# Kernel optimization log

Hardware: AMD Instinct MI355X
Metric: run time of the kernel (lower is better)

## Reference

```python
import jax, jax.numpy as jnp
import numpy as np

N_CELLS = 4096          # rows of sparse x
N_INPUT_GENES = 20000   # cols of sparse x == len(input_gene_list)
N_PRETRAINED = 30000    # rows of embedding table
NUM_HID = 128
NNZ = 2097152           # ~512 expressed genes per cell


def setup_inputs() -> dict:
    key = jax.random.key(0)
    k_val, k_row, k_col, k_gidx, k_emb = jax.random.split(key, 5)
    x_values = jax.random.uniform(k_val, (NNZ,), dtype=jnp.float32)
    x_rows = jnp.sort(jax.random.randint(k_row, (NNZ,), 0, N_CELLS))
    x_cols = jax.random.randint(k_col, (NNZ,), 0, N_INPUT_GENES)
    gene_idx = jax.random.randint(k_gidx, (N_INPUT_GENES,), 0, N_PRETRAINED)
    # nn.Parameter(torch.randn(...) * 0.005)
    embs = jax.random.normal(k_emb, (N_PRETRAINED, NUM_HID), dtype=jnp.float32) * 0.005
    return {"x_values": x_values, "x_rows": x_rows, "x_cols": x_cols,
            "gene_idx": gene_idx, "embs": embs}


def reference(x_values, x_rows, x_cols, gene_idx, embs):
    # feat = F.embedding(gene_idx, embs)           -> [G_in, H]
    # out  = torch.sparse.mm(x, feat)              -> [N_cells, H]
    # Fused: gather per-nnz embedding rows, scale by value, segment-sum by cell.
    feat = embs[gene_idx]                                   # [G_in, H]
    contrib = x_values[:, None] * feat[x_cols]              # [NNZ, H]
    out = jax.ops.segment_sum(contrib, x_rows,
                              num_segments=N_CELLS,
                              indices_are_sorted=True)      # [N_cells, H]
    return out
```

## Files before the change

kernel.cpp:

```cpp
#include <hip/hip_runtime.h>

#define NNZ_TOT    2097152
#define N_CELLS    4096
#define N_GIN      20000
#define N_PRE      30000
#define NUM_HID    128

#define GA_OFF    0
#define GA_BYTES  ((((size_t)NNZ_TOT * 2) + 255) & ~(size_t)255)
#define E8_OFF    (GA_OFF + GA_BYTES)
#define E8_BYTES  ((size_t)N_PRE * NUM_HID)
#define RS_OFF    (E8_OFF + E8_BYTES)
#define RS_BYTES  ((((size_t)N_PRE * 4) + 255) & ~(size_t)255)
#define RP_OFF    (RS_OFF + RS_BYTES)
#define RP_BYTES  ((((size_t)(N_CELLS + 1) * 4) + 255) & ~(size_t)255)
#define WS_NEED   (RP_OFF + RP_BYTES)

#define NB_GA ((NNZ_TOT + 255) / 256)
#define NB_RP ((N_CELLS + 256) / 256)

__global__ __launch_bounds__(256) void precompute_kernel(
    const int* __restrict__ xc, const int* __restrict__ gidx,
    const int* __restrict__ xr, unsigned short* __restrict__ ga,
    int* __restrict__ rp)
{
    const int b = blockIdx.x;
    if (b < NB_GA) {
        const int i = b * 256 + threadIdx.x;
        if (i < NNZ_TOT) ga[i] = (unsigned short)gidx[xc[i]];
    } else {
        const int r = (b - NB_GA) * 256 + threadIdx.x;
        if (r <= N_CELLS) {
            int lo = 0, hi = NNZ_TOT;
            while (lo < hi) {
                const int mid = (lo + hi) >> 1;
                if (xr[mid] < r) lo = mid + 1; else hi = mid;
            }
            rp[r] = lo;
        }
    }
}

__global__ __launch_bounds__(256) void convert_embs8_kernel(
    const float* __restrict__ embs, unsigned char* __restrict__ e8,
    float* __restrict__ rs)
{
    const int row  = (blockIdx.x * blockDim.x + threadIdx.x) >> 6;
    const int lane = threadIdx.x & 63;
    if (row >= N_PRE) return;
    const long base = (long)row * NUM_HID;
    const float e0 = embs[base + lane];
    const float e1 = embs[base + 64 + lane];
    float m = fmaxf(fabsf(e0), fabsf(e1));
    for (int d = 1; d < 64; d <<= 1) m = fmaxf(m, __shfl_xor(m, d));
    const float sinv = (m > 0.f) ? 127.0f / m : 0.f;
    int b0 = (int)rintf(e0 * sinv) + 128;
    int b1 = (int)rintf(e1 * sinv) + 128;
    b0 = min(max(b0, 0), 255);
    b1 = min(max(b1, 0), 255);
    e8[base + lane]      = (unsigned char)b0;
    e8[base + 64 + lane] = (unsigned char)b1;
    if (lane == 0) rs[row] = m * (1.0f / 127.0f);
}

#define U2F0(w) ((float)((w) & 0xffu))
#define U2F1(w) ((float)(((w) >> 8)  & 0xffu))
#define U2F2(w) ((float)(((w) >> 16) & 0xffu))
#define U2F3(w) ((float)(((w) >> 24) & 0xffu))

__device__ __forceinline__ void fma16i(uint4 f, float vv,
                                       float4& a0, float4& a1,
                                       float4& a2, float4& a3, float& S) {
    a0.x = fmaf(vv, U2F0(f.x), a0.x);
    a0.y = fmaf(vv, U2F1(f.x), a0.y);
    a0.z = fmaf(vv, U2F2(f.x), a0.z);
    a0.w = fmaf(vv, U2F3(f.x), a0.w);
    a1.x = fmaf(vv, U2F0(f.y), a1.x);
    a1.y = fmaf(vv, U2F1(f.y), a1.y);
    a1.z = fmaf(vv, U2F2(f.y), a1.z);
    a1.w = fmaf(vv, U2F3(f.y), a1.w);
    a2.x = fmaf(vv, U2F0(f.z), a2.x);
    a2.y = fmaf(vv, U2F1(f.z), a2.y);
    a2.z = fmaf(vv, U2F2(f.z), a2.z);
    a2.w = fmaf(vv, U2F3(f.z), a2.w);
    a3.x = fmaf(vv, U2F0(f.w), a3.x);
    a3.y = fmaf(vv, U2F1(f.w), a3.y);
    a3.z = fmaf(vv, U2F2(f.w), a3.z);
    a3.w = fmaf(vv, U2F3(f.w), a3.w);
    S += vv;
}

__global__ __launch_bounds__(256) void omics_row8_kernel(
    const float*          __restrict__ xv,
    const unsigned short* __restrict__ ga,
    const int*            __restrict__ rp,
    const unsigned int*   __restrict__ e8,
    const float*          __restrict__ rs,
    float*                __restrict__ out)
{
    const int wave = (blockIdx.x * blockDim.x + threadIdx.x) >> 6;
    const int lane = threadIdx.x & 63;
    const int sub  = lane & 7;
    const int oct  = lane >> 3;
    const int r    = __builtin_amdgcn_readfirstlane(wave);
    if (r >= N_CELLS) return;

    const uint4* __restrict__ ebq = reinterpret_cast<const uint4*>(e8);

    const int lo = rp[r];
    const int hi = rp[r + 1];

    float4 a0 = make_float4(0.f,0.f,0.f,0.f), a1 = a0, a2 = a0, a3 = a0;
    float4 b0 = a0, b1 = a0, b2 = a0, b3 = a0;
    float Sa = 0.f, Sb = 0.f;

    int i = lo;
    for (; i + 64 <= hi; i += 64) {
        const int i0 = i + oct;
        const int g0 = ga[i0];      const float w0 = xv[i0]      * rs[g0];
        const int g1 = ga[i0 + 8];  const float w1 = xv[i0 + 8]  * rs[g1];
        const int g2 = ga[i0 + 16]; const float w2 = xv[i0 + 16] * rs[g2];
        const int g3 = ga[i0 + 24]; const float w3 = xv[i0 + 24] * rs[g3];
        const int g4 = ga[i0 + 32]; const float w4 = xv[i0 + 32] * rs[g4];
        const int g5 = ga[i0 + 40]; const float w5 = xv[i0 + 40] * rs[g5];
        const int g6 = ga[i0 + 48]; const float w6 = xv[i0 + 48] * rs[g6];
        const int g7 = ga[i0 + 56]; const float w7 = xv[i0 + 56] * rs[g7];

        const uint4 f0 = ebq[(long)g0 * 8 + sub];
        const uint4 f1 = ebq[(long)g1 * 8 + sub];
        const uint4 f2 = ebq[(long)g2 * 8 + sub];
        const uint4 f3 = ebq[(long)g3 * 8 + sub];
        const uint4 f4 = ebq[(long)g4 * 8 + sub];
        const uint4 f5 = ebq[(long)g5 * 8 + sub];
        const uint4 f6 = ebq[(long)g6 * 8 + sub];
        const uint4 f7 = ebq[(long)g7 * 8 + sub];

        fma16i(f0, w0, a0, a1, a2, a3, Sa);
        fma16i(f1, w1, b0, b1, b2, b3, Sb);
        fma16i(f2, w2, a0, a1, a2, a3, Sa);
        fma16i(f3, w3, b0, b1, b2, b3, Sb);
        fma16i(f4, w4, a0, a1, a2, a3, Sa);
        fma16i(f5, w5, b0, b1, b2, b3, Sb);
        fma16i(f6, w6, a0, a1, a2, a3, Sa);
        fma16i(f7, w7, b0, b1, b2, b3, Sb);
    }
    for (; i < hi; i += 8) {
        const int  idx = i + oct;
        const bool ok  = idx < hi;
        const int   gg = ga[ok ? idx : lo];
        const float vv = ok ? xv[idx] * rs[gg] : 0.f;
        const uint4 f  = ebq[(long)gg * 8 + sub];
        fma16i(f, vv, a0, a1, a2, a3, Sa);
    }

    a0.x += b0.x; a0.y += b0.y; a0.z += b0.z; a0.w += b0.w;
    a1.x += b1.x; a1.y += b1.y; a1.z += b1.z; a1.w += b1.w;
    a2.x += b2.x; a2.y += b2.y; a2.z += b2.z; a2.w += b2.w;
    a3.x += b3.x; a3.y += b3.y; a3.z += b3.z; a3.w += b3.w;
    Sa += Sb;

    #define RED(c) c += __shfl_xor(c, 8); c += __shfl_xor(c, 16); c += __shfl_xor(c, 32)
    RED(a0.x); RED(a0.y); RED(a0.z); RED(a0.w);
    RED(a1.x); RED(a1.y); RED(a1.z); RED(a1.w);
    RED(a2.x); RED(a2.y); RED(a2.z); RED(a2.w);
    RED(a3.x); RED(a3.y); RED(a3.z); RED(a3.w);
    RED(Sa);
    #undef RED

    if (oct == 0) {
        const float c = 128.0f * Sa;
        float* o = &out[(long)r * NUM_HID + sub * 16];
        *reinterpret_cast<float4*>(o)      = make_float4(a0.x-c, a0.y-c, a0.z-c, a0.w-c);
        *reinterpret_cast<float4*>(o + 4)  = make_float4(a1.x-c, a1.y-c, a1.z-c, a1.w-c);
        *reinterpret_cast<float4*>(o + 8)  = make_float4(a2.x-c, a2.y-c, a2.z-c, a2.w-c);
        *reinterpret_cast<float4*>(o + 12) = make_float4(a3.x-c, a3.y-c, a3.z-c, a3.w-c);
    }
}

__global__ __launch_bounds__(256) void omics_fp32_row_kernel(
    const float* __restrict__ xv, const int* __restrict__ xr,
    const int* __restrict__ xc, const int* __restrict__ gidx,
    const float* __restrict__ embs, float* __restrict__ out)
{
    const int wave = (blockIdx.x * blockDim.x + threadIdx.x) >> 6;
    const int lane = threadIdx.x & 63;
    if (wave >= N_CELLS) return;
    int lo = 0, hi = NNZ_TOT;
    while (lo < hi) { int m = (lo + hi) >> 1; if (xr[m] < wave) lo = m + 1; else hi = m; }
    int lo2 = lo, hi2 = NNZ_TOT;
    while (lo2 < hi2) { int m = (lo2 + hi2) >> 1; if (xr[m] < wave + 1) lo2 = m + 1; else hi2 = m; }
    const int h = lane * 2;
    float2 acc = make_float2(0.f, 0.f);
    for (int i = lo; i < lo2; ++i) {
        const float v = xv[i];
        const int   g = gidx[xc[i]];
        const float2 f = *reinterpret_cast<const float2*>(&embs[(long)g * NUM_HID + h]);
        acc.x = fmaf(v, f.x, acc.x);
        acc.y = fmaf(v, f.y, acc.y);
    }
    *reinterpret_cast<float2*>(&out[(long)wave * NUM_HID + h]) = acc;
}

extern "C" void kernel_launch(void* const* d_in, const int* in_sizes, int n_in,
                              void* d_out, int out_size, void* d_ws, size_t ws_size,
                              hipStream_t stream) {
    const float* xv   = (const float*)d_in[0];
    const int*   xr   = (const int*)  d_in[1];
    const int*   xc   = (const int*)  d_in[2];
    const int*   gidx = (const int*)  d_in[3];
    const float* embs = (const float*)d_in[4];
    float*       out  = (float*)d_out;

    if (ws_size >= WS_NEED) {
        unsigned short* ga = (unsigned short*)((char*)d_ws + GA_OFF);
        unsigned char*  e8 = (unsigned char*)((char*)d_ws + E8_OFF);
        float*          rs = (float*)((char*)d_ws + RS_OFF);
        int*            rp = (int*)((char*)d_ws + RP_OFF);

        precompute_kernel<<<NB_GA + NB_RP, 256, 0, stream>>>(xc, gidx, xr, ga, rp);
        convert_embs8_kernel<<<(N_PRE * 64 + 255) / 256, 256, 0, stream>>>(
            embs, e8, rs);

        omics_row8_kernel<<<(N_CELLS * 64) / 256, 256, 0, stream>>>(
            xv, ga, rp, (const unsigned int*)e8, rs, out);
    } else {
        omics_fp32_row_kernel<<<(N_CELLS * 64) / 256, 256, 0, stream>>>(
            xv, xr, xc, gidx, embs, out);
    }
}
```

Measured before the change: 123.4 us.

## Precompute per-nnz scaled weights and merge embedding quantization with row-pointer search

Moves the per-nnz multiply of the value by the row scale (an extra gather of rs) out of the main row kernel into a vectorized prep kernel that writes a float weight array alongside the gene indices. The embedding int8 conversion is rewritten to process two rows per wave with float4 loads and packed 32-bit stores, and it is merged with the row-pointer binary search into one launch. The main kernel then streams precomputed weights instead of doing a dependent rs lookup, at the cost of an extra 8 MB workspace write and read.

```diff
diff --git a/kernel.cpp b/kernel.cpp
--- a/kernel.cpp
+++ b/kernel.cpp
@@ -8,7 +8,9 @@
 
 #define GA_OFF    0
 #define GA_BYTES  ((((size_t)NNZ_TOT * 2) + 255) & ~(size_t)255)
-#define E8_OFF    (GA_OFF + GA_BYTES)
+#define WV_OFF    (GA_OFF + GA_BYTES)
+#define WV_BYTES  ((size_t)NNZ_TOT * 4)
+#define E8_OFF    (WV_OFF + WV_BYTES)
 #define E8_BYTES  ((size_t)N_PRE * NUM_HID)
 #define RS_OFF    (E8_OFF + E8_BYTES)
 #define RS_BYTES  ((((size_t)N_PRE * 4) + 255) & ~(size_t)255)
@@ -16,20 +18,41 @@
 #define RP_BYTES  ((((size_t)(N_CELLS + 1) * 4) + 255) & ~(size_t)255)
 #define WS_NEED   (RP_OFF + RP_BYTES)
 
-#define NB_GA ((NNZ_TOT + 255) / 256)
+#define NB_CV (N_PRE / 8)
 #define NB_RP ((N_CELLS + 256) / 256)
 
-__global__ __launch_bounds__(256) void precompute_kernel(
-    const int* __restrict__ xc, const int* __restrict__ gidx,
-    const int* __restrict__ xr, unsigned short* __restrict__ ga,
+__global__ __launch_bounds__(256) void convert_kernel(
+    const float* __restrict__ embs, const int* __restrict__ xr,
+    unsigned int* __restrict__ e8w, float* __restrict__ rs,
     int* __restrict__ rp)
 {
     const int b = blockIdx.x;
-    if (b < NB_GA) {
-        const int i = b * 256 + threadIdx.x;
-        if (i < NNZ_TOT) ga[i] = (unsigned short)gidx[xc[i]];
+    if (b < NB_CV) {
+        const int wid  = b * 4 + ((int)threadIdx.x >> 6);
+        const int lane = threadIdx.x & 63;
+        const int half = lane >> 5;
+        const int q    = lane & 31;
+        const int row  = wid * 2 + half;
+        if (row >= N_PRE) return;
+        const float4 e = *reinterpret_cast<const float4*>(
+            &embs[(long)row * NUM_HID + q * 4]);
+        float m = fmaxf(fmaxf(fabsf(e.x), fabsf(e.y)),
+                        fmaxf(fabsf(e.z), fabsf(e.w)));
+        m = fmaxf(m, __shfl_xor(m, 1));
+        m = fmaxf(m, __shfl_xor(m, 2));
+        m = fmaxf(m, __shfl_xor(m, 4));
+        m = fmaxf(m, __shfl_xor(m, 8));
+        m = fmaxf(m, __shfl_xor(m, 16));
+        const float sinv = (m > 0.f) ? 127.0f / m : 0.f;
+        int b0 = min(max((int)rintf(e.x * sinv) + 128, 0), 255);
+        int b1 = min(max((int)rintf(e.y * sinv) + 128, 0), 255);
+        int b2 = min(max((int)rintf(e.z * sinv) + 128, 0), 255);
+        int b3 = min(max((int)rintf(e.w * sinv) + 128, 0), 255);
+        e8w[row * 32 + q] = (unsigned)b0 | ((unsigned)b1 << 8) |
+                            ((unsigned)b2 << 16) | ((unsigned)b3 << 24);
+        if (q == 0) rs[row] = m * (1.0f / 127.0f);
     } else {
-        const int r = (b - NB_GA) * 256 + threadIdx.x;
+        const int r = (b - NB_CV) * 256 + threadIdx.x;
         if (r <= N_CELLS) {
             int lo = 0, hi = NNZ_TOT;
             while (lo < hi) {
@@ -41,26 +64,28 @@
     }
 }
 
-__global__ __launch_bounds__(256) void convert_embs8_kernel(
-    const float* __restrict__ embs, unsigned char* __restrict__ e8,
-    float* __restrict__ rs)
-{
-    const int row  = (blockIdx.x * blockDim.x + threadIdx.x) >> 6;
-    const int lane = threadIdx.x & 63;
-    if (row >= N_PRE) return;
-    const long base = (long)row * NUM_HID;
-    const float e0 = embs[base + lane];
-    const float e1 = embs[base + 64 + lane];
-    float m = fmaxf(fabsf(e0), fabsf(e1));
-    for (int d = 1; d < 64; d <<= 1) m = fmaxf(m, __shfl_xor(m, d));
-    const float sinv = (m > 0.f) ? 127.0f / m : 0.f;
-    int b0 = (int)rintf(e0 * sinv) + 128;
-    int b1 = (int)rintf(e1 * sinv) + 128;
-    b0 = min(max(b0, 0), 255);
-    b1 = min(max(b1, 0), 255);
-    e8[base + lane]      = (unsigned char)b0;
-    e8[base + 64 + lane] = (unsigned char)b1;
-    if (lane == 0) rs[row] = m * (1.0f / 127.0f);
+#define NB_PREP (NNZ_TOT / 4 / 256)
+
+__global__ __launch_bounds__(256) void prep_kernel(
+    const float* __restrict__ xv, const int* __restrict__ xc,
+    const int* __restrict__ gidx, const float* __restrict__ rs,
+    unsigned short* __restrict__ ga, float* __restrict__ wv)
+{
+    const long i = ((long)blockIdx.x * 256 + threadIdx.x) * 4;
+    if (i < NNZ_TOT) {
+        const int4   c4 = *reinterpret_cast<const int4*>(&xc[i]);
+        const float4 v4 = *reinterpret_cast<const float4*>(&xv[i]);
+        const int g0 = gidx[c4.x], g1 = gidx[c4.y];
+        const int g2 = gidx[c4.z], g3 = gidx[c4.w];
+        ushort4 g;
+        g.x = (unsigned short)g0; g.y = (unsigned short)g1;
+        g.z = (unsigned short)g2; g.w = (unsigned short)g3;
+        *reinterpret_cast<ushort4*>(&ga[i]) = g;
+        float4 w;
+        w.x = v4.x * rs[g0]; w.y = v4.y * rs[g1];
+        w.z = v4.z * rs[g2]; w.w = v4.w * rs[g3];
+        *reinterpret_cast<float4*>(&wv[i]) = w;
+    }
 }
 
 #define U2F0(w) ((float)((w) & 0xffu))
@@ -91,11 +116,10 @@
 }
 
 __global__ __launch_bounds__(256) void omics_row8_kernel(
-    const float*          __restrict__ xv,
+    const float*          __restrict__ wv,
     const unsigned short* __restrict__ ga,
     const int*            __restrict__ rp,
     const unsigned int*   __restrict__ e8,
-    const float*          __restrict__ rs,
     float*                __restrict__ out)
 {
     const int wave = (blockIdx.x * blockDim.x + threadIdx.x) >> 6;
@@ -117,14 +141,14 @@
     int i = lo;
     for (; i + 64 <= hi; i += 64) {
         const int i0 = i + oct;
-        const int g0 = ga[i0];      const float w0 = xv[i0]      * rs[g0];
-        const int g1 = ga[i0 + 8];  const float w1 = xv[i0 + 8]  * rs[g1];
-        const int g2 = ga[i0 + 16]; const float w2 = xv[i0 + 16] * rs[g2];
-        const int g3 = ga[i0 + 24]; const float w3 = xv[i0 + 24] * rs[g3];
-        const int g4 = ga[i0 + 32]; const float w4 = xv[i0 + 32] * rs[g4];
-        const int g5 = ga[i0 + 40]; const float w5 = xv[i0 + 40] * rs[g5];
-        const int g6 = ga[i0 + 48]; const float w6 = xv[i0 + 48] * rs[g6];
-        const int g7 = ga[i0 + 56]; const float w7 = xv[i0 + 56] * rs[g7];
+        const int g0 = ga[i0];      const float w0 = wv[i0];
+        const int g1 = ga[i0 + 8];  const float w1 = wv[i0 + 8];
+        const int g2 = ga[i0 + 16]; const float w2 = wv[i0 + 16];
+        const int g3 = ga[i0 + 24]; const float w3 = wv[i0 + 24];
+        const int g4 = ga[i0 + 32]; const float w4 = wv[i0 + 32];
+        const int g5 = ga[i0 + 40]; const float w5 = wv[i0 + 40];
+        const int g6 = ga[i0 + 48]; const float w6 = wv[i0 + 48];
+        const int g7 = ga[i0 + 56]; const float w7 = wv[i0 + 56];
 
         const uint4 f0 = ebq[(long)g0 * 8 + sub];
         const uint4 f1 = ebq[(long)g1 * 8 + sub];
@@ -148,7 +172,7 @@
         const int  idx = i + oct;
         const bool ok  = idx < hi;
         const int   gg = ga[ok ? idx : lo];
-        const float vv = ok ? xv[idx] * rs[gg] : 0.f;
+        const float vv = ok ? wv[idx] : 0.f;
         const uint4 f  = ebq[(long)gg * 8 + sub];
         fma16i(f, vv, a0, a1, a2, a3, Sa);
     }
@@ -213,16 +237,16 @@
 
     if (ws_size >= WS_NEED) {
         unsigned short* ga = (unsigned short*)((char*)d_ws + GA_OFF);
-        unsigned char*  e8 = (unsigned char*)((char*)d_ws + E8_OFF);
+        float*          wv = (float*)((char*)d_ws + WV_OFF);
+        unsigned int*   e8 = (unsigned int*)((char*)d_ws + E8_OFF);
         float*          rs = (float*)((char*)d_ws + RS_OFF);
         int*            rp = (int*)((char*)d_ws + RP_OFF);
 
-        precompute_kernel<<<NB_GA + NB_RP, 256, 0, stream>>>(xc, gidx, xr, ga, rp);
-        convert_embs8_kernel<<<(N_PRE * 64 + 255) / 256, 256, 0, stream>>>(
-            embs, e8, rs);
+        convert_kernel<<<NB_CV + NB_RP, 256, 0, stream>>>(embs, xr, e8, rs, rp);
+        prep_kernel<<<NB_PREP, 256, 0, stream>>>(xv, xc, gidx, rs, ga, wv);
 
         omics_row8_kernel<<<(N_CELLS * 64) / 256, 256, 0, stream>>>(
-            xv, ga, rp, (const unsigned int*)e8, rs, out);
+            wv, ga, rp, e8, out);
     } else {
         omics_fp32_row_kernel<<<(N_CELLS * 64) / 256, 256, 0, stream>>>(
             xv, xr, xc, gidx, embs, out);
```

Result: slower. 128.0 us (+3.7%).
